# Performance work log

Measured on AMD Instinct MI355X. Metric: run time of the kernel, lower is better.

The kernel has to match this reference:

```python
import jax, jax.numpy as jnp
import numpy as np

D_MODEL = 1024
N_HEADS = 16
HEAD_DIM = D_MODEL // N_HEADS


def rotate_half(x):
    # interleaved rotate: (-x_odd, x_even) re-interleaved
    x1 = x[..., ::2]
    x2 = x[..., 1::2]
    return jnp.stack((-x2, x1), axis=-1).reshape(x.shape)


def rope_tables(seq_len, dim, dtype):
    inv_freq = 1.0 / (10000.0 ** (jnp.arange(0, dim, 2, dtype=jnp.float32) / dim))
    t = jnp.arange(seq_len, dtype=jnp.float32)
    freqs = jnp.einsum('i,j->ij', t, inv_freq)          # [T, dim/2]
    emb = jnp.concatenate((freqs, freqs), axis=-1)       # [T, dim]
    return jnp.cos(emb).astype(dtype)[None, None], jnp.sin(emb).astype(dtype)[None, None]


def setup_inputs() -> dict:
    key = jax.random.key(0)
    k1, k2, k3 = jax.random.split(key, 3)
    B, T, C = 2, 2048, D_MODEL
    scale_in = 1.0 / np.sqrt(C)
    return {
        'x': jax.random.normal(k1, (B, T, C), dtype=jnp.float32),
        'attention_mask': jnp.ones((B, T), dtype=jnp.int32),
        'qkv_w': jax.random.normal(k2, (3 * C, C), dtype=jnp.float32) * scale_in,
        'qkv_b': jnp.zeros((3 * C,), dtype=jnp.float32),
        'out_w': jax.random.normal(k3, (C, C), dtype=jnp.float32) * scale_in,
        'out_b': jnp.zeros((C,), dtype=jnp.float32),
    }


def reference(x, attention_mask, qkv_w, qkv_b, out_w, out_b):
    B, T, C = x.shape
    H, Dh = N_HEADS, HEAD_DIM
    qkv = x @ qkv_w.T + qkv_b                             # [B,T,3C]
    q, k, v = jnp.split(qkv, 3, axis=-1)
    q = q.reshape(B, T, H, Dh).transpose(0, 2, 1, 3)      # [B,H,T,Dh]
    k = k.reshape(B, T, H, Dh).transpose(0, 2, 1, 3)
    v = v.reshape(B, T, H, Dh).transpose(0, 2, 1, 3)
    cos, sin = rope_tables(T, Dh, x.dtype)                # [1,1,T,Dh]
    q = q * cos + rotate_half(q) * sin
    k = k * cos + rotate_half(k) * sin
    att = jnp.einsum('bhqd,bhkd->bhqk', q, k) / jnp.sqrt(jnp.array(Dh, x.dtype))
    causal = jnp.tril(jnp.ones((T, T), dtype=bool))[None, None]
    key_mask = attention_mask.astype(bool)[:, None, None, :]
    neg_inf = jnp.array(-jnp.inf, att.dtype)
    att = jnp.where(causal & key_mask, att, neg_inf)
    att = jax.nn.softmax(att, axis=-1)
    query_mask = attention_mask.astype(bool)[:, None, :, None]
    att = att * query_mask
    y = jnp.einsum('bhqk,bhkd->bhqd', att, v)             # [B,H,T,Dh]
    y = y.transpose(0, 2, 1, 3).reshape(B, T, C)
    y = y * attention_mask[:, :, None].astype(y.dtype)
    y = y @ out_w.T + out_b
    return y
```

## Files before the change

kernel.cpp:

```cpp
#include <hip/hip_runtime.h>
#include <hip/hip_bf16.h>

typedef __bf16 bf16;
typedef __bf16 bf16x4 __attribute__((ext_vector_type(4)));
typedef __bf16 bf16x8 __attribute__((ext_vector_type(8)));
typedef float f32x4 __attribute__((ext_vector_type(4)));
typedef unsigned int u32x4 __attribute__((ext_vector_type(4)));

#define T_LEN 2048
#define NHEAD 16
#define DHEAD 64
#define CDIM 1024
#define NB 2

__device__ __forceinline__ void g2l16(const void* g, void* l) {
    __builtin_amdgcn_global_load_lds(
        (const __attribute__((address_space(1))) unsigned int*)g,
        (__attribute__((address_space(3))) unsigned int*)l, 16, 0, 0);
}

__device__ __forceinline__ float fexp2(float x) {
    float r;
    asm("v_exp_f32 %0, %1" : "=v"(r) : "v"(x));
    return r;
}

__device__ __forceinline__ void stage_swz512(const bf16* __restrict__ g, size_t gstride,
                                             bf16* lds, int t) {
    int off = t * 16;
    int row = off >> 7;
    int lcol = (off & 127) ^ ((row & 7) << 4);
    g2l16(g + (size_t)row * gstride + (lcol >> 1), (char*)lds + off);
}

__device__ __forceinline__ bf16x8 rd_swz(const bf16* lds, int row, int colB) {
    return *(const bf16x8*)((const char*)lds + row * 128 + (colB ^ ((row & 7) << 4)));
}

__global__ __launch_bounds__(256) void prep_kernel(
    const float* __restrict__ x, const float* __restrict__ qkv_w,
    const float* __restrict__ out_w, const int* __restrict__ am,
    bf16* __restrict__ xb, bf16* __restrict__ wqb, bf16* __restrict__ wob,
    float* __restrict__ ct, float* __restrict__ st, float* __restrict__ mf,
    int* __restrict__ mflag) {
    int bid = blockIdx.x;
    if (bid < 4096) {
        int i = bid * 256 + threadIdx.x;
        const float* src; bf16* dst; int j;
        if (i < 524288)      { src = x;     dst = xb;  j = i; }
        else if (i < 917504) { src = qkv_w; dst = wqb; j = i - 524288; }
        else                 { src = out_w; dst = wob; j = i - 917504; }
        const float4* p = (const float4*)src + (size_t)j * 2;
        float4 a = p[0], b = p[1];
        bf16x8 o;
        o[0] = (bf16)a.x; o[1] = (bf16)a.y; o[2] = (bf16)a.z; o[3] = (bf16)a.w;
        o[4] = (bf16)b.x; o[5] = (bf16)b.y; o[6] = (bf16)b.z; o[7] = (bf16)b.w;
        ((bf16x8*)dst)[j] = o;
    } else if (bid < 4608) {
        int i = (bid - 4096) * 256 + threadIdx.x;
        int t = i >> 6, d = i & 63;
        float ex = (float)(2 * (d & 31)) / 64.0f;
        float inv = powf(10000.0f, -ex);
        float ang = (float)t * inv;
        ct[i] = cosf(ang);
        st[i] = sinf(ang);
    } else {
        int i = (bid - 4608) * 256 + threadIdx.x;
        int v = am[i];
        mf[i] = (v != 0) ? 0.0f : -1e30f;
        unsigned long long bz = __ballot(v == 0);
        if ((threadIdx.x & 63) == 0) mflag[i >> 6] = (bz != 0) ? 1 : 0;
    }
}

__global__ __launch_bounds__(256) void gemm_qkv_kernel(
    const bf16* __restrict__ xb, const bf16* __restrict__ wb,
    const float* __restrict__ bias,
    const float* __restrict__ ct, const float* __restrict__ st,
    bf16* __restrict__ qg, bf16* __restrict__ kg, bf16* __restrict__ vt) {
    __shared__ __align__(16) bf16 smem[2 * 128 * 64];
    bf16* sA = smem;
    bf16* sB = smem + 128 * 64;
    int m0 = blockIdx.x * 128, n0 = blockIdx.y * 128;
    int t = threadIdx.x, w = t >> 6, l = t & 63;
    int wm = w >> 1, wn = w & 1;
    int l15 = l & 15, lhi = l >> 4;
    f32x4 acc[4][4] = {};
    for (int k0 = 0; k0 < CDIM; k0 += 64) {
#pragma unroll
        for (int i = 0; i < 4; i++) {
            int off = i * 4096 + t * 16;
            int row = off >> 7;
            int lcol = (off & 127) ^ ((row & 7) << 4);
            g2l16(xb + (size_t)(m0 + row) * CDIM + k0 + (lcol >> 1), (char*)sA + off);
            g2l16(wb + (size_t)(n0 + row) * CDIM + k0 + (lcol >> 1), (char*)sB + off);
        }
        __syncthreads();
#pragma unroll
        for (int ks = 0; ks < 2; ks++) {
            bf16x8 af[4], bfr[4];
#pragma unroll
            for (int mt = 0; mt < 4; mt++)
                af[mt] = rd_swz(sA, wm * 64 + mt * 16 + l15, ks * 64 + lhi * 16);
#pragma unroll
            for (int nt = 0; nt < 4; nt++)
                bfr[nt] = rd_swz(sB, wn * 64 + nt * 16 + l15, ks * 64 + lhi * 16);
#pragma unroll
            for (int mt = 0; mt < 4; mt++)
#pragma unroll
                for (int nt = 0; nt < 4; nt++)
                    acc[mt][nt] = __builtin_amdgcn_mfma_f32_16x16x32_bf16(
                        af[mt], bfr[nt], acc[mt][nt], 0, 0, 0);
        }
        __syncthreads();
    }
    int bb = m0 >> 11, tt0 = m0 & 2047;
    if (n0 >= 2048) {
        bf16* sT = smem;
#pragma unroll
        for (int pass = 0; pass < 2; pass++) {
            __syncthreads();
            if (wn == pass) {
#pragma unroll
                for (int nt = 0; nt < 4; nt++) {
                    float cb = bias[n0 + pass * 64 + nt * 16 + l15];
#pragma unroll
                    for (int mt = 0; mt < 4; mt++) {
                        bf16x4 pv;
#pragma unroll
                        for (int r = 0; r < 4; r++) pv[r] = (bf16)(acc[mt][nt][r] + cb);
                        *(bf16x4*)(sT + (nt * 16 + l15) * 136 + wm * 64 + mt * 16 + lhi * 4) = pv;
                    }
                }
            }
            __syncthreads();
            int h_p = ((n0 & 1023) >> 6) + pass;
            size_t vbase = ((size_t)(bb * NHEAD + h_p)) * T_LEN * DHEAD + tt0;
#pragma unroll
            for (int c = 0; c < 4; c++) {
                int cid = c * 256 + t;
                int d = cid >> 4, ch = cid & 15;
                *(bf16x8*)(vt + vbase + (size_t)d * T_LEN + ch * 8) =
                    *(const bf16x8*)(sT + d * 136 + ch * 8);
            }
        }
        return;
    }
    int sec = n0 >> 10;
    bf16* og = (sec == 0) ? qg : kg;
    float oscale = (sec == 0) ? 0.125f * 1.44269504f : 1.0f;
#pragma unroll
    for (int nt = 0; nt < 4; nt++) {
        int col = n0 + wn * 64 + nt * 16 + l15;
        int cc = col & 1023;
        int h = cc >> 6, d = cc & 63;
        float cb = bias[col];
        size_t hb = ((size_t)(bb * NHEAD + h)) * T_LEN * DHEAD;
#pragma unroll
        for (int mt = 0; mt < 4; mt++) {
#pragma unroll
            for (int r = 0; r < 4; r++) {
                int tt = tt0 + wm * 64 + mt * 16 + lhi * 4 + r;
                float v = acc[mt][nt][r] + cb;
                float p = __shfl_xor(v, 1);
                float cs = ct[tt * 64 + d], sn = st[tt * 64 + d];
                float o = (d & 1) ? (v * cs + p * sn) : (v * cs - p * sn);
                og[hb + (size_t)tt * DHEAD + d] = (bf16)(o * oscale);
            }
        }
    }
}

__global__ __launch_bounds__(512, 4) void attn_kernel(
    const bf16* __restrict__ qg, const bf16* __restrict__ kg, const bf16* __restrict__ vt,
    const float* __restrict__ maskf, const int* __restrict__ mflag,
    bf16* __restrict__ yb) {
    __shared__ __align__(16) bf16 sK[2][64 * 64];
    __shared__ __align__(16) bf16 sV[2][64 * 64];
    int lin = blockIdx.x;
    int xcd = lin & 7, idx = lin >> 3;
    int group = idx >> 4, pos = idx & 15;
    int qt0 = (pos & 1) ? (pos >> 1) : (15 - (pos >> 1));
    int qt = (group & 2) ? (15 - qt0) : qt0;
    int pair = xcd * 4 + group;
    int h = pair & 15, b = pair >> 4;
    int q0 = qt * 128;
    int t = threadIdx.x, w = t >> 6, l = t & 63;
    int l15 = l & 15, lhi = l >> 4;
    const size_t head_off = ((size_t)(b * NHEAD + h)) * T_LEN * DHEAD;
    const bf16* qb = qg + head_off;
    const bf16* kb = kg + head_off;
    const bf16* vb = vt + head_off;
    const float* mrow = maskf + b * T_LEN;
    const int* mfl = mflag + b * (T_LEN / 64);
    const int wq0 = q0 + w * 16;
    const int qrow_l = wq0 + l15;
    bf16x8 qf[2];
    {
        qf[0] = *(const bf16x8*)(qb + (size_t)qrow_l * DHEAD + lhi * 8);
        qf[1] = *(const bf16x8*)(qb + (size_t)qrow_l * DHEAD + 32 + lhi * 8);
    }
    const u32x4 onesu = {0x3F803F80u, 0x3F803F80u, 0x3F803F80u, 0x3F803F80u};
    const bf16x8 ones8 = __builtin_bit_cast(bf16x8, onesu);
    float m_ = -1e30f;
    f32x4 lsv = {};
    f32x4 accy[4] = {};
    stage_swz512(kb, DHEAD, sK[0], t);
    stage_swz512(vb, T_LEN, sV[0], t);
    __syncthreads();
    int cur = 0;
    const int kv_end = q0 + 64;
    for (int kv0 = 0; kv0 <= kv_end; kv0 += 64) {
        if (kv0 + 64 <= kv_end) {
            stage_swz512(kb + (size_t)(kv0 + 64) * DHEAD, DHEAD, sK[cur ^ 1], t);
            stage_swz512(vb + (kv0 + 64), T_LEN, sV[cur ^ 1], t);
        }
        if (kv0 <= wq0 + 15) {
            f32x4 s[4] = {};
            __builtin_amdgcn_s_setprio(1);
#pragma unroll
            for (int c = 0; c < 4; c++)
#pragma unroll
                for (int ks = 0; ks < 2; ks++) {
                    bf16x8 kf = rd_swz(sK[cur], c * 16 + l15, ks * 64 + lhi * 16);
                    s[c] = __builtin_amdgcn_mfma_f32_16x16x32_bf16(kf, qf[ks], s[c], 0, 0, 0);
                }
            __builtin_amdgcn_s_setprio(0);
            bool diag = (kv0 + 63 > wq0);
            int needmask = mfl[kv0 >> 6];
            float mxl = -1e30f;
            if (!needmask && !diag) {
#pragma unroll
                for (int c = 0; c < 4; c++)
#pragma unroll
                    for (int r = 0; r < 4; r++) mxl = fmaxf(mxl, s[c][r]);
            } else {
#pragma unroll
                for (int c = 0; c < 4; c++) {
                    float mpv[4] = {0.f, 0.f, 0.f, 0.f};
                    if (needmask) {
                        float4 mq = *(const float4*)(mrow + kv0 + c * 16 + lhi * 4);
                        mpv[0] = mq.x; mpv[1] = mq.y; mpv[2] = mq.z; mpv[3] = mq.w;
                    }
#pragma unroll
                    for (int r = 0; r < 4; r++) {
                        float sv = s[c][r] + mpv[r];
                        if (diag && (kv0 + c * 16 + lhi * 4 + r > qrow_l)) sv = -1e30f;
                        s[c][r] = sv;
                        mxl = fmaxf(mxl, sv);
                    }
                }
            }
            float mx = fmaxf(mxl, __shfl_xor(mxl, 16));
            mx = fmaxf(mx, __shfl_xor(mx, 32));
            if (kv0 == 0) m_ = mx;
#pragma unroll
            for (int c = 0; c < 4; c++)
#pragma unroll
                for (int r = 0; r < 4; r++) s[c][r] = fexp2(s[c][r] - m_);
            if (kv0 != 0 && !__all(mx <= m_ + 8.f)) {
                float mn = fmaxf(m_, mx);
                float scf = fexp2(m_ - mn);
                m_ = mn;
#pragma unroll
                for (int c = 0; c < 4; c++)
#pragma unroll
                    for (int r = 0; r < 4; r++) s[c][r] *= scf;
#pragma unroll
                for (int r = 0; r < 4; r++) {
                    float sr = __shfl(scf, (l & 48) + lhi * 4 + r);
                    lsv[r] *= sr;
#pragma unroll
                    for (int dt = 0; dt < 4; dt++) accy[dt][r] *= sr;
                }
            }
            __builtin_amdgcn_s_setprio(1);
#pragma unroll
            for (int g2 = 0; g2 < 2; g2++) {
                unsigned a0, a1, b0, b1;
                asm("v_cvt_pk_bf16_f32 %0, %1, %2" : "=v"(a0) : "v"(s[2 * g2][0]), "v"(s[2 * g2][1]));
                asm("v_cvt_pk_bf16_f32 %0, %1, %2" : "=v"(a1) : "v"(s[2 * g2][2]), "v"(s[2 * g2][3]));
                asm("v_cvt_pk_bf16_f32 %0, %1, %2" : "=v"(b0) : "v"(s[2 * g2 + 1][0]), "v"(s[2 * g2 + 1][1]));
                asm("v_cvt_pk_bf16_f32 %0, %1, %2" : "=v"(b1) : "v"(s[2 * g2 + 1][2]), "v"(s[2 * g2 + 1][3]));
                asm("v_permlane32_swap_b32 %0, %1" : "+v"(a0), "+v"(b0));
                asm("v_permlane16_swap_b32 %0, %1" : "+v"(a0), "+v"(b0));
                asm("v_permlane32_swap_b32 %0, %1" : "+v"(a1), "+v"(b1));
                asm("v_permlane16_swap_b32 %0, %1" : "+v"(a1), "+v"(b1));
                u32x4 pu;
                pu[0] = a0; pu[1] = a1; pu[2] = b0; pu[3] = b1;
                bf16x8 pv = __builtin_bit_cast(bf16x8, pu);
                lsv = __builtin_amdgcn_mfma_f32_16x16x32_bf16(pv, ones8, lsv, 0, 0, 0);
#pragma unroll
                for (int dt = 0; dt < 4; dt++) {
                    bf16x8 vf = rd_swz(sV[cur], dt * 16 + l15, g2 * 64 + lhi * 16);
                    accy[dt] = __builtin_amdgcn_mfma_f32_16x16x32_bf16(pv, vf, accy[dt], 0, 0, 0);
                }
            }
            __builtin_amdgcn_s_setprio(0);
        }
        __syncthreads();
        cur ^= 1;
    }
#pragma unroll
    for (int r = 0; r < 4; r++) {
        float inv = lsv[r] > 0.f ? 1.0f / lsv[r] : 0.0f;
        int rowt = wq0 + lhi * 4 + r;
        size_t obase = ((size_t)(b * T_LEN + rowt)) * CDIM + (size_t)h * DHEAD;
#pragma unroll
        for (int dt = 0; dt < 4; dt++)
            yb[obase + dt * 16 + l15] = (bf16)(accy[dt][r] * inv);
    }
}

__global__ __launch_bounds__(256) void gemm_out_kernel(
    const bf16* __restrict__ yb, const bf16* __restrict__ wb,
    const float* __restrict__ bias, float* __restrict__ out) {
    __shared__ __align__(16) bf16 sA[128 * 64];
    __shared__ __align__(16) bf16 sB[64 * 64];
    int m0 = blockIdx.x * 128, n0 = blockIdx.y * 64;
    int t = threadIdx.x, w = t >> 6, l = t & 63;
    int wm = w >> 1, wn = w & 1;
    int l15 = l & 15, lhi = l >> 4;
    f32x4 acc[4][2] = {};
    for (int k0 = 0; k0 < CDIM; k0 += 64) {
#pragma unroll
        for (int i = 0; i < 4; i++) {
            int off = i * 4096 + t * 16;
            int row = off >> 7;
            int lcol = (off & 127) ^ ((row & 7) << 4);
            g2l16(yb + (size_t)(m0 + row) * CDIM + k0 + (lcol >> 1), (char*)sA + off);
            if (i < 2)
                g2l16(wb + (size_t)(n0 + row) * CDIM + k0 + (lcol >> 1), (char*)sB + off);
        }
        __syncthreads();
#pragma unroll
        for (int ks = 0; ks < 2; ks++) {
            bf16x8 af[4], bfr[2];
#pragma unroll
            for (int mt = 0; mt < 4; mt++)
                af[mt] = rd_swz(sA, wm * 64 + mt * 16 + l15, ks * 64 + lhi * 16);
#pragma unroll
            for (int nt = 0; nt < 2; nt++)
                bfr[nt] = rd_swz(sB, wn * 32 + nt * 16 + l15, ks * 64 + lhi * 16);
#pragma unroll
            for (int mt = 0; mt < 4; mt++)
#pragma unroll
                for (int nt = 0; nt < 2; nt++)
                    acc[mt][nt] = __builtin_amdgcn_mfma_f32_16x16x32_bf16(
                        af[mt], bfr[nt], acc[mt][nt], 0, 0, 0);
        }
        __syncthreads();
    }
#pragma unroll
    for (int nt = 0; nt < 2; nt++) {
        int col = n0 + wn * 32 + nt * 16 + l15;
        float cb = bias[col];
#pragma unroll
        for (int mt = 0; mt < 4; mt++) {
#pragma unroll
            for (int r = 0; r < 4; r++) {
                int rowm = m0 + wm * 64 + mt * 16 + lhi * 4 + r;
                out[(size_t)rowm * CDIM + col] = acc[mt][nt][r] + cb;
            }
        }
    }
}

extern "C" void kernel_launch(void* const* d_in, const int* in_sizes, int n_in,
                              void* d_out, int out_size, void* d_ws, size_t ws_size,
                              hipStream_t stream) {
    const float* x      = (const float*)d_in[0];
    const int*   amask  = (const int*)d_in[1];
    const float* qkv_w  = (const float*)d_in[2];
    const float* qkv_b  = (const float*)d_in[3];
    const float* out_w  = (const float*)d_in[4];
    const float* out_b  = (const float*)d_in[5];
    float* out = (float*)d_out;

    char* ws = (char*)d_ws;
    bf16* xb  = (bf16*)(ws);
    bf16* wqb = (bf16*)(ws + (8ull  << 20));
    bf16* wob = (bf16*)(ws + (14ull << 20));
    bf16* qg  = (bf16*)(ws + (16ull << 20));
    bf16* kg  = (bf16*)(ws + (24ull << 20));
    bf16* vt  = (bf16*)(ws + (32ull << 20));
    bf16* yb  = (bf16*)(ws + (40ull << 20));
    float* ctab = (float*)(ws + (48ull << 20));
    float* stab = (float*)(ws + (48ull << 20) + (1ull << 19));
    float* mkf  = (float*)(ws + (49ull << 20));
    int*   mfg  = (int*)(ws + (49ull << 20) + (16ull << 10));

    prep_kernel<<<4624, 256, 0, stream>>>(x, qkv_w, out_w, amask,
                                          xb, wqb, wob, ctab, stab, mkf, mfg);
    gemm_qkv_kernel<<<dim3(32, 24), 256, 0, stream>>>(xb, wqb, qkv_b, ctab, stab, qg, kg, vt);
    attn_kernel<<<dim3(512), 512, 0, stream>>>(qg, kg, vt, mkf, mfg, yb);
    gemm_out_kernel<<<dim3(32, 16), 256, 0, stream>>>(yb, wob, out_b, out);
}
```

Baseline: 114.5 us.

## Shrink QKV GEMM tile to 128x64 and remap blocks per XCD for L2 reuse

```diff
diff --git a/kernel.cpp b/kernel.cpp
--- a/kernel.cpp
+++ b/kernel.cpp
@@ -73,89 +73,91 @@
     }
 }
 
-__global__ __launch_bounds__(256) void gemm_qkv_kernel(
+__global__ __launch_bounds__(256, 6) void gemm_qkv_kernel(
     const bf16* __restrict__ xb, const bf16* __restrict__ wb,
     const float* __restrict__ bias,
     const float* __restrict__ ct, const float* __restrict__ st,
     bf16* __restrict__ qg, bf16* __restrict__ kg, bf16* __restrict__ vt) {
-    __shared__ __align__(16) bf16 smem[2 * 128 * 64];
+    __shared__ __align__(16) bf16 smem[128 * 64 + 64 * 64];
     bf16* sA = smem;
     bf16* sB = smem + 128 * 64;
-    int m0 = blockIdx.x * 128, n0 = blockIdx.y * 128;
+    int lin = blockIdx.x;
+    int xcd = lin & 7, idx = lin >> 3;
+    int xtile = idx & 31, ypanel = idx >> 5;
+    int m0 = xtile * 128, n0 = (xcd * 6 + ypanel) * 64;
     int t = threadIdx.x, w = t >> 6, l = t & 63;
     int wm = w >> 1, wn = w & 1;
     int l15 = l & 15, lhi = l >> 4;
-    f32x4 acc[4][4] = {};
+    f32x4 acc[4][2] = {};
     for (int k0 = 0; k0 < CDIM; k0 += 64) {
 #pragma unroll
-        for (int i = 0; i < 4; i++) {
-            int off = i * 4096 + t * 16;
+        for (int c = 0; c < 4; c++) {
+            int off = c * 4096 + t * 16;
             int row = off >> 7;
             int lcol = (off & 127) ^ ((row & 7) << 4);
             g2l16(xb + (size_t)(m0 + row) * CDIM + k0 + (lcol >> 1), (char*)sA + off);
+        }
+#pragma unroll
+        for (int c = 0; c < 2; c++) {
+            int off = c * 4096 + t * 16;
+            int row = off >> 7;
+            int lcol = (off & 127) ^ ((row & 7) << 4);
             g2l16(wb + (size_t)(n0 + row) * CDIM + k0 + (lcol >> 1), (char*)sB + off);
         }
         __syncthreads();
 #pragma unroll
         for (int ks = 0; ks < 2; ks++) {
-            bf16x8 af[4], bfr[4];
+            bf16x8 af[4], bfr[2];
 #pragma unroll
             for (int mt = 0; mt < 4; mt++)
                 af[mt] = rd_swz(sA, wm * 64 + mt * 16 + l15, ks * 64 + lhi * 16);
 #pragma unroll
-            for (int nt = 0; nt < 4; nt++)
-                bfr[nt] = rd_swz(sB, wn * 64 + nt * 16 + l15, ks * 64 + lhi * 16);
+            for (int nt = 0; nt < 2; nt++)
+                bfr[nt] = rd_swz(sB, wn * 32 + nt * 16 + l15, ks * 64 + lhi * 16);
 #pragma unroll
             for (int mt = 0; mt < 4; mt++)
 #pragma unroll
-                for (int nt = 0; nt < 4; nt++)
+                for (int nt = 0; nt < 2; nt++)
                     acc[mt][nt] = __builtin_amdgcn_mfma_f32_16x16x32_bf16(
                         af[mt], bfr[nt], acc[mt][nt], 0, 0, 0);
         }
         __syncthreads();
     }
     int bb = m0 >> 11, tt0 = m0 & 2047;
+    int h = (n0 & 1023) >> 6;
     if (n0 >= 2048) {
         bf16* sT = smem;
 #pragma unroll
-        for (int pass = 0; pass < 2; pass++) {
-            __syncthreads();
-            if (wn == pass) {
-#pragma unroll
-                for (int nt = 0; nt < 4; nt++) {
-                    float cb = bias[n0 + pass * 64 + nt * 16 + l15];
-#pragma unroll
-                    for (int mt = 0; mt < 4; mt++) {
-                        bf16x4 pv;
-#pragma unroll
-                        for (int r = 0; r < 4; r++) pv[r] = (bf16)(acc[mt][nt][r] + cb);
-                        *(bf16x4*)(sT + (nt * 16 + l15) * 136 + wm * 64 + mt * 16 + lhi * 4) = pv;
-                    }
-                }
-            }
-            __syncthreads();
-            int h_p = ((n0 & 1023) >> 6) + pass;
-            size_t vbase = ((size_t)(bb * NHEAD + h_p)) * T_LEN * DHEAD + tt0;
-#pragma unroll
-            for (int c = 0; c < 4; c++) {
-                int cid = c * 256 + t;
-                int d = cid >> 4, ch = cid & 15;
-                *(bf16x8*)(vt + vbase + (size_t)d * T_LEN + ch * 8) =
-                    *(const bf16x8*)(sT + d * 136 + ch * 8);
-            }
+        for (int nt = 0; nt < 2; nt++) {
+            int dl = wn * 32 + nt * 16 + l15;
+            float cb = bias[n0 + dl];
+#pragma unroll
+            for (int mt = 0; mt < 4; mt++) {
+                bf16x4 pv;
+#pragma unroll
+                for (int r = 0; r < 4; r++) pv[r] = (bf16)(acc[mt][nt][r] + cb);
+                *(bf16x4*)(sT + dl * 136 + wm * 64 + mt * 16 + lhi * 4) = pv;
+            }
+        }
+        __syncthreads();
+        size_t vbase = ((size_t)(bb * NHEAD + h)) * T_LEN * DHEAD + tt0;
+#pragma unroll
+        for (int c = 0; c < 4; c++) {
+            int cid = c * 256 + t;
+            int d = cid >> 4, ch = cid & 15;
+            *(bf16x8*)(vt + vbase + (size_t)d * T_LEN + ch * 8) =
+                *(const bf16x8*)(sT + d * 136 + ch * 8);
         }
         return;
     }
     int sec = n0 >> 10;
     bf16* og = (sec == 0) ? qg : kg;
     float oscale = (sec == 0) ? 0.125f * 1.44269504f : 1.0f;
-#pragma unroll
-    for (int nt = 0; nt < 4; nt++) {
-        int col = n0 + wn * 64 + nt * 16 + l15;
-        int cc = col & 1023;
-        int h = cc >> 6, d = cc & 63;
-        float cb = bias[col];
-        size_t hb = ((size_t)(bb * NHEAD + h)) * T_LEN * DHEAD;
+    size_t hb = ((size_t)(bb * NHEAD + h)) * T_LEN * DHEAD;
+#pragma unroll
+    for (int nt = 0; nt < 2; nt++) {
+        int d = wn * 32 + nt * 16 + l15;
+        float cb = bias[n0 + d];
 #pragma unroll
         for (int mt = 0; mt < 4; mt++) {
 #pragma unroll
@@ -317,7 +319,10 @@
     const float* __restrict__ bias, float* __restrict__ out) {
     __shared__ __align__(16) bf16 sA[128 * 64];
     __shared__ __align__(16) bf16 sB[64 * 64];
-    int m0 = blockIdx.x * 128, n0 = blockIdx.y * 64;
+    int lin = blockIdx.x;
+    int xcd = lin & 7, idx = lin >> 3;
+    int xtile = idx & 31, ypanel = idx >> 5;
+    int m0 = xtile * 128, n0 = (xcd * 2 + ypanel) * 64;
     int t = threadIdx.x, w = t >> 6, l = t & 63;
     int wm = w >> 1, wn = w & 1;
     int l15 = l & 15, lhi = l >> 4;
@@ -392,7 +397,7 @@
 
     prep_kernel<<<4624, 256, 0, stream>>>(x, qkv_w, out_w, amask,
                                           xb, wqb, wob, ctab, stab, mkf, mfg);
-    gemm_qkv_kernel<<<dim3(32, 24), 256, 0, stream>>>(xb, wqb, qkv_b, ctab, stab, qg, kg, vt);
+    gemm_qkv_kernel<<<1536, 256, 0, stream>>>(xb, wqb, qkv_b, ctab, stab, qg, kg, vt);
     attn_kernel<<<dim3(512), 512, 0, stream>>>(qg, kg, vt, mkf, mfg, yb);
-    gemm_out_kernel<<<dim3(32, 16), 256, 0, stream>>>(yb, wob, out_b, out);
-}
+    gemm_out_kernel<<<512, 256, 0, stream>>>(yb, wob, out_b, out);
+}
```

New measurement: 119.2 us. 1.04x slower.
